# Kernel tuning notes

Hardware: AMD Instinct MI355X
Metric: run time of the kernel (lower is better)

Reference implementation:

```python
import jax, jax.numpy as jnp
import numpy as np

# Module constants (from init_kwargs)
WIN = 256      # window_size
STRIDE = 128   # stride (overlapping windows -> merge averages overlaps)
HEADS = 16


def setup_inputs() -> dict:
    key = jax.random.key(0)
    ks = jax.random.split(key, 5)
    B, S, D = 4, 4096, 1024
    scale = 0.02
    return {
        "hidden_states": jax.random.normal(ks[0], (B, S, D), jnp.float32),
        "Wq": jax.random.normal(ks[1], (D, D), jnp.float32) * scale,
        "Wk": jax.random.normal(ks[2], (D, D), jnp.float32) * scale,
        "Wv": jax.random.normal(ks[3], (D, D), jnp.float32) * scale,
        "Wo": jax.random.normal(ks[4], (D, D), jnp.float32) * scale,
    }


def reference(hidden_states, Wq, Wk, Wv, Wo):
    B, S, D = hidden_states.shape
    H = HEADS
    dh = D // H
    nw = (S - WIN) // STRIDE + 1  # number of sliding windows

    # gather overlapping windows: idx[w, j] = w*STRIDE + j
    idx = jnp.arange(nw)[:, None] * STRIDE + jnp.arange(WIN)[None, :]
    win = hidden_states[:, idx]

    # per-window multi-head attention (mask within a window is all-visible)
    def proj(x, Wm):
        return jnp.einsum('bnwd,de->bnwe', x, Wm).reshape(B, nw, WIN, H, dh)

    q = proj(win, Wq)
    k = proj(win, Wk)
    v = proj(win, Wv)

    scores = jnp.einsum('bnqhd,bnkhd->bnhqk', q, k) / jnp.sqrt(jnp.asarray(dh, q.dtype))
    attn = jax.nn.softmax(scores, axis=-1)
    ctx = jnp.einsum('bnhqk,bnkhd->bnqhd', attn, v)
    ctx = ctx.reshape(B, nw, WIN, D)
    win_out = jnp.einsum('bnwd,de->bnwe', ctx, Wo)

    # scatter-merge with overlap averaging
    flat_idx = idx.reshape(-1)
    out = jnp.zeros((B, S, D), hidden_states.dtype).at[:, flat_idx].add(
        win_out.reshape(B, nw * WIN, D))
    count = jnp.zeros((S,), hidden_states.dtype).at[flat_idx].add(1.0)
    out = out / (count[None, :, None] + 1e-8)
    return out
```

## Files before the change

kernel.cpp:

```cpp
#include <hip/hip_runtime.h>

#define SEQ 4096
#define DIM 1024
#define NWIN 31
#define NHEAD 16
#define NT 16

typedef __attribute__((ext_vector_type(8))) short bf16x8;
typedef __attribute__((ext_vector_type(4))) float f32x4;

#define MFMA(a, b, c) __builtin_amdgcn_mfma_f32_16x16x32_bf16((a), (b), (c), 0, 0, 0)

__device__ __forceinline__ unsigned short f2bf(float f) {
  union { float f; unsigned u; } v; v.f = f;
  unsigned r = v.u + 0x7FFFu + ((v.u >> 16) & 1u);
  return (unsigned short)(r >> 16);
}
__device__ __forceinline__ float bf2f(unsigned short h) {
  union { unsigned u; float f; } v; v.u = ((unsigned)h) << 16;
  return v.f;
}
__device__ __forceinline__ unsigned cvtpk(float lo, float hi) {
  unsigned r;
  asm("v_cvt_pk_bf16_f32 %0, %1, %2" : "=v"(r) : "v"(lo), "v"(hi));
  return r;
}
__device__ __forceinline__ unsigned addbf2(unsigned x, unsigned y) {
  union { unsigned u; float f; } a, b, c, d;
  a.u = x << 16; b.u = x & 0xffff0000u;
  c.u = y << 16; d.u = y & 0xffff0000u;
  return cvtpk(a.f + c.f, b.f + d.f);
}

__device__ __forceinline__ void gll16(const void* g, void* l) {
  __builtin_amdgcn_global_load_lds((const __attribute__((address_space(1))) unsigned*)g,
                                   (__attribute__((address_space(3))) unsigned*)l,
                                   16, 0, 0);
}


__global__ __launch_bounds__(256) void cast_x_k(const float* __restrict__ x,
                                                unsigned short* __restrict__ o) {
  size_t i = ((size_t)blockIdx.x * 256 + threadIdx.x) * 8;
  float4 a = *(const float4*)(x + i);
  float4 b = *(const float4*)(x + i + 4);
  union { unsigned short u[8]; uint4 v; } pk;
  pk.u[0] = f2bf(a.x); pk.u[1] = f2bf(a.y); pk.u[2] = f2bf(a.z); pk.u[3] = f2bf(a.w);
  pk.u[4] = f2bf(b.x); pk.u[5] = f2bf(b.y); pk.u[6] = f2bf(b.z); pk.u[7] = f2bf(b.w);
  *(uint4*)(o + i) = pk.v;
}

__global__ __launch_bounds__(256) void zero_ctxb_k(unsigned short* __restrict__ ctxB) {
  int gtid = blockIdx.x * 256 + threadIdx.x;
  int idx = gtid * 8;
  int srow = idx >> 10;
  int b = srow >> 8;
  int r = srow & 255;
  int seqrow = b * SEQ + ((r < 128) ? r : (3840 + r));
  uint4 z = {0, 0, 0, 0};
  *(uint4*)(ctxB + (size_t)seqrow * DIM + (idx & 1023)) = z;
}


__global__ __launch_bounds__(256) void tcast_w_k(const float* __restrict__ W0, const float* __restrict__ W1,
                                                 const float* __restrict__ W2, const float* __restrict__ W3,
                                                 unsigned short* __restrict__ Wt3,
                                                 unsigned short* __restrict__ WoT) {
  __shared__ float tile[64][65];
  const int bid = blockIdx.x;
  const int mat = bid >> 8;
  const int t = bid & 255;
  const int tr = (t >> 4) * 64, tc = (t & 15) * 64;
  const float* W = (mat == 0) ? W0 : (mat == 1) ? W1 : (mat == 2) ? W2 : W3;
  unsigned short* out = (mat < 3) ? (Wt3 + (size_t)mat * 1024 * 1024) : WoT;
  const float fscale = (mat == 0) ? 0.18033688011112042f : 1.0f;
  const int tid = threadIdx.x;
  const int rr = tid >> 4, cc = (tid & 15) << 2;
#pragma unroll
  for (int i = 0; i < 4; ++i) {
    int r = i * 16 + rr;
    float4 v = *(const float4*)(W + (size_t)(tr + r) * DIM + tc + cc);
    tile[r][cc] = v.x; tile[r][cc + 1] = v.y; tile[r][cc + 2] = v.z; tile[r][cc + 3] = v.w;
  }
  __syncthreads();
#pragma unroll
  for (int i = 0; i < 4; ++i) {
    int orow = i * 16 + rr;
    union { unsigned short u[4]; uint2 v; } pk;
#pragma unroll
    for (int j = 0; j < 4; ++j) pk.u[j] = f2bf(tile[cc + j][orow] * fscale);
    *(uint2*)(out + (size_t)(tc + orow) * DIM + tr + cc) = pk.v;
  }
}


__device__ __forceinline__ void stage_half(const unsigned short* __restrict__ src,
                                           int row0, int kcol0, char* slot, int tid) {
  const int w = tid >> 6;
  const int r0 = tid >> 2;
  const int c = (((tid & 3) ^ ((tid >> 3) & 3))) * 8;
  gll16(src + (size_t)(row0 + r0) * DIM + kcol0 + c, slot + w * 1024);
  gll16(src + (size_t)(row0 + 128 + r0) * DIM + kcol0 + c, slot + 8192 + w * 1024);
}

__device__ __forceinline__ void gemm256_core(const unsigned short* __restrict__ A,
                                             const unsigned short* __restrict__ Bt,
                                             int m0, int n0, char* lds,
                                             f32x4 acc[8][4], int tid) {
  const int lane = tid & 63, w = tid >> 6;
  const int wm = w >> 2, wn = w & 3;
  const int l15 = lane & 15, g = lane >> 4;
  const int gs = g ^ ((l15 >> 1) & 3);

#define ASLOT(b, kk) (lds + ((b) * 2 + (kk)) * 16384)
#define BSLOT(b, kk) (lds + 65536 + ((b) * 2 + (kk)) * 16384)

  const int aoff = (wm * 128 + l15) * 64 + gs * 16;
  const int boff = (wn * 64 + l15) * 64 + gs * 16;

  stage_half(A,  m0, 0,  ASLOT(0, 0), tid);
  stage_half(Bt, n0, 0,  BSLOT(0, 0), tid);
  stage_half(A,  m0, 32, ASLOT(0, 1), tid);
  stage_half(Bt, n0, 32, BSLOT(0, 1), tid);
  stage_half(A,  m0, 64, ASLOT(1, 0), tid);
  stage_half(Bt, n0, 64, BSLOT(1, 0), tid);
  asm volatile("s_waitcnt vmcnt(8)" ::: "memory");
  __builtin_amdgcn_s_barrier();

  for (int s = 0; s < NT; ++s) {
    const int b = s & 1, nb = b ^ 1;
    const int k1 = (s + 1 < NT ? s + 1 : NT - 1) * 64;
    const int k2 = (s + 2 < NT ? s + 2 : NT - 1) * 64;
    char* Ab0 = ASLOT(b, 0); char* Ab1 = ASLOT(b, 1);
    char* Bb0 = BSLOT(b, 0); char* Bb1 = BSLOT(b, 1);
    bf16x8 af[8], bq0, bq1;

#pragma unroll
    for (int mt = 0; mt < 8; ++mt) af[mt] = *(const bf16x8*)(Ab0 + aoff + mt * 1024);
    bq0 = *(const bf16x8*)(Bb0 + boff);
    bq1 = *(const bf16x8*)(Bb0 + boff + 1024);
    stage_half(A, m0, k1 + 32, ASLOT(nb, 1), tid);
    __builtin_amdgcn_s_barrier();
    __builtin_amdgcn_s_setprio(1);
#pragma unroll
    for (int mt = 0; mt < 8; ++mt) {
      acc[mt][0] = MFMA(af[mt], bq0, acc[mt][0]);
      acc[mt][1] = MFMA(af[mt], bq1, acc[mt][1]);
    }
    __builtin_amdgcn_s_setprio(0);

    bq0 = *(const bf16x8*)(Bb0 + boff + 2048);
    bq1 = *(const bf16x8*)(Bb0 + boff + 3072);
    stage_half(Bt, n0, k1 + 32, BSLOT(nb, 1), tid);
    asm volatile("s_waitcnt vmcnt(8)" ::: "memory");
    __builtin_amdgcn_s_barrier();
    __builtin_amdgcn_s_setprio(1);
#pragma unroll
    for (int mt = 0; mt < 8; ++mt) {
      acc[mt][2] = MFMA(af[mt], bq0, acc[mt][2]);
      acc[mt][3] = MFMA(af[mt], bq1, acc[mt][3]);
    }
    __builtin_amdgcn_s_setprio(0);

#pragma unroll
    for (int mt = 0; mt < 8; ++mt) af[mt] = *(const bf16x8*)(Ab1 + aoff + mt * 1024);
    bq0 = *(const bf16x8*)(Bb1 + boff);
    bq1 = *(const bf16x8*)(Bb1 + boff + 1024);
    stage_half(A, m0, k2, ASLOT(b, 0), tid);
    __builtin_amdgcn_s_barrier();
    __builtin_amdgcn_s_setprio(1);
#pragma unroll
    for (int mt = 0; mt < 8; ++mt) {
      acc[mt][0] = MFMA(af[mt], bq0, acc[mt][0]);
      acc[mt][1] = MFMA(af[mt], bq1, acc[mt][1]);
    }
    __builtin_amdgcn_s_setprio(0);

    bq0 = *(const bf16x8*)(Bb1 + boff + 2048);
    bq1 = *(const bf16x8*)(Bb1 + boff + 3072);
    stage_half(Bt, n0, k2, BSLOT(b, 0), tid);
    asm volatile("s_waitcnt vmcnt(8)" ::: "memory");
    __builtin_amdgcn_s_barrier();
    __builtin_amdgcn_s_setprio(1);
#pragma unroll
    for (int mt = 0; mt < 8; ++mt) {
      acc[mt][2] = MFMA(af[mt], bq0, acc[mt][2]);
      acc[mt][3] = MFMA(af[mt], bq1, acc[mt][3]);
    }
    __builtin_amdgcn_s_setprio(0);
  }
#undef ASLOT
#undef BSLOT
}


struct AR { uint4 a0, b0, a1, b1; };

__device__ __forceinline__ void issueA(const unsigned short* __restrict__ cA,
                                       const unsigned short* __restrict__ cB,
                                       int row0, int kcol0, int tid, AR& r) {
  const int r0 = tid >> 2;
  const int c = (((tid & 3) ^ ((tid >> 3) & 3))) * 8;
  const size_t o1 = (size_t)(row0 + r0) * DIM + kcol0 + c;
  const size_t o2 = (size_t)(row0 + 128 + r0) * DIM + kcol0 + c;
  r.a0 = *(const uint4*)(cA + o1);
  r.b0 = *(const uint4*)(cB + o1);
  r.a1 = *(const uint4*)(cA + o2);
  r.b1 = *(const uint4*)(cB + o2);
}

__device__ __forceinline__ void writeA(char* slot, int tid, const AR& r) {
  uint4 lo, hi;
  lo.x = addbf2(r.a0.x, r.b0.x); lo.y = addbf2(r.a0.y, r.b0.y);
  lo.z = addbf2(r.a0.z, r.b0.z); lo.w = addbf2(r.a0.w, r.b0.w);
  hi.x = addbf2(r.a1.x, r.b1.x); hi.y = addbf2(r.a1.y, r.b1.y);
  hi.z = addbf2(r.a1.z, r.b1.z); hi.w = addbf2(r.a1.w, r.b1.w);
  *(uint4*)(slot + tid * 16) = lo;
  *(uint4*)(slot + 8192 + tid * 16) = hi;
}

__device__ __forceinline__ void gemm256_core_sum(const unsigned short* __restrict__ cA,
                                                 const unsigned short* __restrict__ cB,
                                                 const unsigned short* __restrict__ Bt,
                                                 int m0, int n0, char* lds,
                                                 f32x4 acc[8][4], int tid) {
  const int lane = tid & 63, w = tid >> 6;
  const int wm = w >> 2, wn = w & 3;
  const int l15 = lane & 15, g = lane >> 4;
  const int gs = g ^ ((l15 >> 1) & 3);

#define ASLOT(b, kk) (lds + ((b) * 2 + (kk)) * 16384)
#define BSLOT(b, kk) (lds + 65536 + ((b) * 2 + (kk)) * 16384)

  const int aoff = (wm * 128 + l15) * 64 + gs * 16;
  const int boff = (wn * 64 + l15) * 64 + gs * 16;

  AR R0, R1;
  issueA(cA, cB, m0, 0, tid, R0);  writeA(ASLOT(0, 0), tid, R0);
  issueA(cA, cB, m0, 32, tid, R0); writeA(ASLOT(0, 1), tid, R0);
  issueA(cA, cB, m0, 64, tid, R0); writeA(ASLOT(1, 0), tid, R0);
  stage_half(Bt, n0, 0,  BSLOT(0, 0), tid);
  stage_half(Bt, n0, 32, BSLOT(0, 1), tid);
  stage_half(Bt, n0, 64, BSLOT(1, 0), tid);
  issueA(cA, cB, m0, 96, tid, R1);
  asm volatile("s_waitcnt vmcnt(8)" ::: "memory");
  asm volatile("s_waitcnt lgkmcnt(0)" ::: "memory");
  __builtin_amdgcn_s_barrier();

  for (int s = 0; s < NT; ++s) {
    const int b = s & 1, nb = b ^ 1;
    const int k1 = (s + 1 < NT ? s + 1 : NT - 1) * 64;
    const int k2 = (s + 2 < NT ? s + 2 : NT - 1) * 64;
    char* Ab0 = ASLOT(b, 0); char* Ab1 = ASLOT(b, 1);
    char* Bb0 = BSLOT(b, 0); char* Bb1 = BSLOT(b, 1);
    bf16x8 af[8], bq0, bq1;
    (void)k1;

    writeA(ASLOT(nb, 1), tid, R1);
    asm volatile("s_waitcnt lgkmcnt(0)" ::: "memory");
    issueA(cA, cB, m0, k2, tid, R0);
#pragma unroll
    for (int mt = 0; mt < 8; ++mt) af[mt] = *(const bf16x8*)(Ab0 + aoff + mt * 1024);
    bq0 = *(const bf16x8*)(Bb0 + boff);
    bq1 = *(const bf16x8*)(Bb0 + boff + 1024);
    __builtin_amdgcn_s_barrier();
    __builtin_amdgcn_s_setprio(1);
#pragma unroll
    for (int mt = 0; mt < 8; ++mt) {
      acc[mt][0] = MFMA(af[mt], bq0, acc[mt][0]);
      acc[mt][1] = MFMA(af[mt], bq1, acc[mt][1]);
    }
    __builtin_amdgcn_s_setprio(0);

    bq0 = *(const bf16x8*)(Bb0 + boff + 2048);
    bq1 = *(const bf16x8*)(Bb0 + boff + 3072);
    stage_half(Bt, n0, k1 + 32, BSLOT(nb, 1), tid);
    asm volatile("s_waitcnt vmcnt(8)" ::: "memory");
    __builtin_amdgcn_s_barrier();
    __builtin_amdgcn_s_setprio(1);
#pragma unroll
    for (int mt = 0; mt < 8; ++mt) {
      acc[mt][2] = MFMA(af[mt], bq0, acc[mt][2]);
      acc[mt][3] = MFMA(af[mt], bq1, acc[mt][3]);
    }
    __builtin_amdgcn_s_setprio(0);

    writeA(ASLOT(b, 0), tid, R0);
    asm volatile("s_waitcnt lgkmcnt(0)" ::: "memory");
    issueA(cA, cB, m0, k2 + 32, tid, R1);
#pragma unroll
    for (int mt = 0; mt < 8; ++mt) af[mt] = *(const bf16x8*)(Ab1 + aoff + mt * 1024);
    bq0 = *(const bf16x8*)(Bb1 + boff);
    bq1 = *(const bf16x8*)(Bb1 + boff + 1024);
    __builtin_amdgcn_s_barrier();
    __builtin_amdgcn_s_setprio(1);
#pragma unroll
    for (int mt = 0; mt < 8; ++mt) {
      acc[mt][0] = MFMA(af[mt], bq0, acc[mt][0]);
      acc[mt][1] = MFMA(af[mt], bq1, acc[mt][1]);
    }
    __builtin_amdgcn_s_setprio(0);

    bq0 = *(const bf16x8*)(Bb1 + boff + 2048);
    bq1 = *(const bf16x8*)(Bb1 + boff + 3072);
    stage_half(Bt, n0, k2, BSLOT(b, 0), tid);
    asm volatile("s_waitcnt vmcnt(8)" ::: "memory");
    __builtin_amdgcn_s_barrier();
    __builtin_amdgcn_s_setprio(1);
#pragma unroll
    for (int mt = 0; mt < 8; ++mt) {
      acc[mt][2] = MFMA(af[mt], bq0, acc[mt][2]);
      acc[mt][3] = MFMA(af[mt], bq1, acc[mt][3]);
    }
    __builtin_amdgcn_s_setprio(0);
  }
#undef ASLOT
#undef BSLOT
}


__global__ __launch_bounds__(512, 2) void gemm_qkv_k(const unsigned short* __restrict__ Xb,
                                                     const unsigned short* __restrict__ Wt3,
                                                     unsigned short* __restrict__ Qb,
                                                     unsigned short* __restrict__ Kb,
                                                     unsigned short* __restrict__ Vt) {
  __shared__ char lds[131072];
  const int nwg = 768;
  const int wg = blockIdx.x;
  const int swz = (wg & 7) * (nwg >> 3) + (wg >> 3);
  const int mtile = swz / 12, ntile = swz % 12;
  const int m0 = mtile * 256, n0 = ntile * 256;
  const int tid = threadIdx.x;

  f32x4 acc[8][4] = {};
  gemm256_core(Xb, Wt3, m0, n0, lds, acc, tid);

  const int lane = tid & 63, w = tid >> 6;
  const int wm = w >> 2, wn = w & 3;
  const int l15 = lane & 15, g = lane >> 4;
  const int mg0 = m0 + wm * 128;
  const int ng0 = n0 + wn * 64;

  if (n0 < 2048) {
    unsigned short* O = (n0 < 1024) ? Qb : Kb;
    const int nb = (n0 < 1024) ? 0 : 1024;
#pragma unroll
    for (int mt = 0; mt < 8; ++mt)
#pragma unroll
      for (int nt = 0; nt < 4; ++nt) {
        int ng = ng0 + nt * 16 + l15 - nb;
        int mg = mg0 + mt * 16 + g * 4;
#pragma unroll
        for (int r = 0; r < 4; ++r)
          O[(size_t)(mg + r) * DIM + ng] = f2bf(acc[mt][nt][r]);
      }
  } else {
#pragma unroll
    for (int mt = 0; mt < 8; ++mt)
#pragma unroll
      for (int nt = 0; nt < 4; ++nt) {
        int ng = ng0 + nt * 16 + l15 - 2048;
        int mg = mg0 + mt * 16 + g * 4;
        union { unsigned short u[4]; uint2 v; } pk;
#pragma unroll
        for (int r = 0; r < 4; ++r) pk.u[r] = f2bf(acc[mt][nt][r]);
        *(uint2*)(Vt + (size_t)ng * (4 * SEQ) + mg) = pk.v;
      }
  }
}


__global__ __launch_bounds__(512, 2) void gemm_out_k(const unsigned short* __restrict__ cA,
                                                     const unsigned short* __restrict__ cB,
                                                     const unsigned short* __restrict__ WoT,
                                                     float* __restrict__ out) {
  __shared__ char lds[131072];
  const int nwg = 256;
  const int wg = blockIdx.x;
  const int swz = (wg & 7) * (nwg >> 3) + (wg >> 3);
  const int mtile = swz >> 2, ntile = swz & 3;
  const int m0 = mtile * 256, n0 = ntile * 256;
  const int tid = threadIdx.x;

  f32x4 acc[8][4] = {};
  gemm256_core_sum(cA, cB, WoT, m0, n0, lds, acc, tid);

  const int lane = tid & 63, w = tid >> 6;
  const int wm = w >> 2, wn = w & 3;
  const int l15 = lane & 15, g = lane >> 4;
  const int mg0 = m0 + wm * 128;
  const int ng0 = n0 + wn * 64;
#pragma unroll
  for (int mt = 0; mt < 8; ++mt)
#pragma unroll
    for (int nt = 0; nt < 4; ++nt) {
      int ng = ng0 + nt * 16 + l15;
      int mg = mg0 + mt * 16 + g * 4;
#pragma unroll
      for (int r = 0; r < 4; ++r) {
        int m = mg + r;
        int s = m & (SEQ - 1);
        float scl = (s < 128 || s >= SEQ - 128) ? 1.0f : 0.5f;
        out[(size_t)m * DIM + ng] = acc[mt][nt][r] * scl;
      }
    }
}


__global__ __launch_bounds__(512, 4) void attn_k(const unsigned short* __restrict__ Qb,
                                                 const unsigned short* __restrict__ Kb,
                                                 const unsigned short* __restrict__ Vt,
                                                 unsigned short* __restrict__ ctxA,
                                                 unsigned short* __restrict__ ctxB) {
  __shared__ char Kls[32768];
  __shared__ char Vls[32768];

  const int bid = blockIdx.x;
  const int h = bid & 15;
  const int rem = bid >> 4;
  const int n = rem % NWIN;
  const int b = rem / NWIN;
  const int tid = threadIdx.x;
  const int lane = tid & 63;
  const int w = tid >> 6;
  const int l15 = lane & 15, g = lane >> 4;

  const size_t qkbase = ((size_t)b * SEQ + (size_t)n * 128) * DIM + h * 64;
  const int wdst = w * 1024;

  {
    const int kr0 = tid >> 3;
    const int ksc = ((tid & 7) ^ (kr0 & 7)) * 8;
    const unsigned short* kg = Kb + qkbase + (size_t)kr0 * DIM + ksc;
#pragma unroll
    for (int j = 0; j < 4; ++j)
      gll16(kg + (size_t)(64 * j) * DIM, Kls + 8192 * j + wdst);
  }
  {
    const int vr0 = tid >> 5;
    const int vsc = ((tid & 31) ^ (vr0 & 7)) * 8;
    const unsigned short* vg = Vt + (size_t)(h * 64 + vr0) * (4 * SEQ) +
                               (size_t)b * SEQ + n * 128 + vsc;
#pragma unroll
    for (int j = 0; j < 4; ++j)
      gll16(vg + (size_t)(16 * j) * (4 * SEQ), Vls + 8192 * j + wdst);
  }

  bf16x8 qf[2][2];
#pragma unroll
  for (int qt = 0; qt < 2; ++qt)
#pragma unroll
    for (int kf = 0; kf < 2; ++kf)
      qf[qt][kf] = *(const bf16x8*)(Qb + qkbase +
                                    (size_t)(w * 32 + qt * 16 + l15) * DIM + kf * 32 + g * 8);

  __syncthreads();

  f32x4 acc[2][4] = {};
  f32x4 psv[2] = {};

  for (int kc = 0; kc < 4; ++kc) {
    f32x4 s0[4] = {}, s1[4] = {};
    __builtin_amdgcn_s_setprio(1);
#pragma unroll
    for (int kt = 0; kt < 4; ++kt) {
      int row = kc * 64 + kt * 16 + l15;
      bf16x8 k0 = *(const bf16x8*)(Kls + row * 128 + ((g ^ (row & 7)) << 4));
      bf16x8 k1 = *(const bf16x8*)(Kls + row * 128 + (((4 + g) ^ (row & 7)) << 4));
      s0[kt] = MFMA(k0, qf[0][0], s0[kt]);
      s0[kt] = MFMA(k1, qf[0][1], s0[kt]);
      s1[kt] = MFMA(k0, qf[1][0], s1[kt]);
      s1[kt] = MFMA(k1, qf[1][1], s1[kt]);
    }
    __builtin_amdgcn_s_setprio(0);
#pragma unroll
    for (int kt = 0; kt < 4; ++kt) {
#pragma unroll
      for (int r = 0; r < 4; ++r) {
        s0[kt][r] = exp2f(s0[kt][r]);
        s1[kt][r] = exp2f(s1[kt][r]);
      }
      psv[0] += s0[kt];
      psv[1] += s1[kt];
    }
    union { unsigned u[4]; bf16x8 v; } pa[2][2];
#pragma unroll
    for (int c = 0; c < 2; ++c) {
      pa[0][c].u[0] = cvtpk(s0[2 * c][0], s0[2 * c][1]);
      pa[0][c].u[1] = cvtpk(s0[2 * c][2], s0[2 * c][3]);
      pa[0][c].u[2] = cvtpk(s0[2 * c + 1][0], s0[2 * c + 1][1]);
      pa[0][c].u[3] = cvtpk(s0[2 * c + 1][2], s0[2 * c + 1][3]);
      pa[1][c].u[0] = cvtpk(s1[2 * c][0], s1[2 * c][1]);
      pa[1][c].u[1] = cvtpk(s1[2 * c][2], s1[2 * c][3]);
      pa[1][c].u[2] = cvtpk(s1[2 * c + 1][0], s1[2 * c + 1][1]);
      pa[1][c].u[3] = cvtpk(s1[2 * c + 1][2], s1[2 * c + 1][3]);
    }
    __builtin_amdgcn_s_setprio(1);
#pragma unroll
    for (int c = 0; c < 2; ++c)
#pragma unroll
      for (int dt = 0; dt < 4; ++dt) {
        int row = dt * 16 + l15;
        int c16 = kc * 8 + c * 4 + (g >> 1);
        int off = (g & 1) * 8;
        union { uint2 u2[2]; bf16x8 v; } vv;
        vv.u2[0] = *(const uint2*)(Vls + row * 512 + ((c16 ^ (row & 7)) << 4) + off);
        vv.u2[1] = *(const uint2*)(Vls + row * 512 + (((c16 + 2) ^ (row & 7)) << 4) + off);
        acc[0][dt] = MFMA(vv.v, pa[0][c].v, acc[0][dt]);
        acc[1][dt] = MFMA(vv.v, pa[1][c].v, acc[1][dt]);
      }
    __builtin_amdgcn_s_setprio(0);
  }

  unsigned short* outb = (n & 1) ? ctxB : ctxA;
  const size_t obase = ((size_t)b * SEQ + (size_t)n * 128 + w * 32) * DIM + h * 64;
#pragma unroll
  for (int qt = 0; qt < 2; ++qt) {
    float ps = psv[qt][0] + psv[qt][1] + psv[qt][2] + psv[qt][3];
    ps += __shfl_xor(ps, 16);
    ps += __shfl_xor(ps, 32);
    float inv = 1.0f / ps;
#pragma unroll
    for (int dt = 0; dt < 4; ++dt) {
      union { unsigned short u[4]; uint2 v; } pk;
#pragma unroll
      for (int r = 0; r < 4; ++r) pk.u[r] = f2bf(acc[qt][dt][r] * inv);
      *(uint2*)(outb + obase + (size_t)(qt * 16 + l15) * DIM + dt * 16 + g * 4) = pk.v;
    }
  }
}


extern "C" void kernel_launch(void* const* d_in, const int* in_sizes, int n_in,
                              void* d_out, int out_size, void* d_ws, size_t ws_size,
                              hipStream_t stream) {
  const float* X  = (const float*)d_in[0];
  const float* Wq = (const float*)d_in[1];
  const float* Wk = (const float*)d_in[2];
  const float* Wv = (const float*)d_in[3];
  const float* Wo = (const float*)d_in[4];
  float* out = (float*)d_out;

  char* ws = (char*)d_ws;
  const size_t SZ = (size_t)4 * SEQ * DIM * 2;
  unsigned short* Xb   = (unsigned short*)(ws);
  unsigned short* Wt3  = (unsigned short*)(ws + SZ);
  unsigned short* WoT  = (unsigned short*)(ws + SZ + 6291456);
  unsigned short* Qb   = (unsigned short*)(ws + SZ + 8388608);
  unsigned short* Kb   = (unsigned short*)(ws + 2 * SZ + 8388608);
  unsigned short* Vt   = (unsigned short*)(ws + 3 * SZ + 8388608);
  unsigned short* ctxA = (unsigned short*)(ws + 4 * SZ + 8388608);
  unsigned short* ctxB = (unsigned short*)(ws + 5 * SZ + 8388608);

  zero_ctxb_k<<<512, 256, 0, stream>>>(ctxB);
  cast_x_k<<<8192, 256, 0, stream>>>(X, Xb);
  tcast_w_k<<<1024, 256, 0, stream>>>(Wq, Wk, Wv, Wo, Wt3, WoT);
  gemm_qkv_k<<<768, 512, 0, stream>>>(Xb, Wt3, Qb, Kb, Vt);
  attn_k<<<4 * NWIN * NHEAD, 512, 0, stream>>>(Qb, Kb, Vt, ctxA, ctxB);
  gemm_out_k<<<256, 512, 0, stream>>>(ctxA, ctxB, WoT, out);
}
```

Measured before the change: 251.2 us.

## Restructure GEMM main loop into four quadrant phases with full-K fragment reuse

Reorganizes the inner loop of both GEMM mainloops into four phases, each covering one output quadrant (4 M-tiles by 2 N-tiles) over both K halves, in place of two K-half passes over 8x2 fragments. This cuts register pressure for A fragments and adds explicit lgkmcnt waits and extra barriers around each phase. Global staging is interleaved per phase and the vmcnt thresholds change to match. It risks more barrier overhead and possible LDS race windows if the wait counts are wrong.

```diff
diff --git a/kernel.cpp b/kernel.cpp
--- a/kernel.cpp
+++ b/kernel.cpp
@@ -124,7 +124,7 @@
   stage_half(Bt, n0, 32, BSLOT(0, 1), tid);
   stage_half(A,  m0, 64, ASLOT(1, 0), tid);
   stage_half(Bt, n0, 64, BSLOT(1, 0), tid);
-  asm volatile("s_waitcnt vmcnt(8)" ::: "memory");
+  asm volatile("s_waitcnt vmcnt(4)" ::: "memory");
   __builtin_amdgcn_s_barrier();
 
   for (int s = 0; s < NT; ++s) {
@@ -133,61 +133,84 @@
     const int k2 = (s + 2 < NT ? s + 2 : NT - 1) * 64;
     char* Ab0 = ASLOT(b, 0); char* Ab1 = ASLOT(b, 1);
     char* Bb0 = BSLOT(b, 0); char* Bb1 = BSLOT(b, 1);
-    bf16x8 af[8], bq0, bq1;
-
-#pragma unroll
-    for (int mt = 0; mt < 8; ++mt) af[mt] = *(const bf16x8*)(Ab0 + aoff + mt * 1024);
-    bq0 = *(const bf16x8*)(Bb0 + boff);
-    bq1 = *(const bf16x8*)(Bb0 + boff + 1024);
+    bf16x8 af[4][2], bqA[2][2], bqB[2][2];
+
+#pragma unroll
+    for (int mt = 0; mt < 4; ++mt) {
+      af[mt][0] = *(const bf16x8*)(Ab0 + aoff + mt * 1024);
+      af[mt][1] = *(const bf16x8*)(Ab1 + aoff + mt * 1024);
+    }
+#pragma unroll
+    for (int nt = 0; nt < 2; ++nt) {
+      bqA[nt][0] = *(const bf16x8*)(Bb0 + boff + nt * 1024);
+      bqA[nt][1] = *(const bf16x8*)(Bb1 + boff + nt * 1024);
+    }
     stage_half(A, m0, k1 + 32, ASLOT(nb, 1), tid);
-    __builtin_amdgcn_s_barrier();
-    __builtin_amdgcn_s_setprio(1);
-#pragma unroll
-    for (int mt = 0; mt < 8; ++mt) {
-      acc[mt][0] = MFMA(af[mt], bq0, acc[mt][0]);
-      acc[mt][1] = MFMA(af[mt], bq1, acc[mt][1]);
-    }
-    __builtin_amdgcn_s_setprio(0);
-
-    bq0 = *(const bf16x8*)(Bb0 + boff + 2048);
-    bq1 = *(const bf16x8*)(Bb0 + boff + 3072);
+    asm volatile("s_waitcnt lgkmcnt(8)" ::: "memory");
+    __builtin_amdgcn_s_barrier();
+    asm volatile("s_waitcnt lgkmcnt(0)" ::: "memory");
+    __builtin_amdgcn_s_setprio(1);
+#pragma unroll
+    for (int mt = 0; mt < 4; ++mt)
+#pragma unroll
+      for (int nt = 0; nt < 2; ++nt) {
+        acc[mt][nt] = MFMA(af[mt][0], bqA[nt][0], acc[mt][nt]);
+        acc[mt][nt] = MFMA(af[mt][1], bqA[nt][1], acc[mt][nt]);
+      }
+    __builtin_amdgcn_s_setprio(0);
+    __builtin_amdgcn_s_barrier();
+
+#pragma unroll
+    for (int nt = 0; nt < 2; ++nt) {
+      bqB[nt][0] = *(const bf16x8*)(Bb0 + boff + (nt + 2) * 1024);
+      bqB[nt][1] = *(const bf16x8*)(Bb1 + boff + (nt + 2) * 1024);
+    }
     stage_half(Bt, n0, k1 + 32, BSLOT(nb, 1), tid);
-    asm volatile("s_waitcnt vmcnt(8)" ::: "memory");
-    __builtin_amdgcn_s_barrier();
-    __builtin_amdgcn_s_setprio(1);
-#pragma unroll
-    for (int mt = 0; mt < 8; ++mt) {
-      acc[mt][2] = MFMA(af[mt], bq0, acc[mt][2]);
-      acc[mt][3] = MFMA(af[mt], bq1, acc[mt][3]);
-    }
-    __builtin_amdgcn_s_setprio(0);
-
-#pragma unroll
-    for (int mt = 0; mt < 8; ++mt) af[mt] = *(const bf16x8*)(Ab1 + aoff + mt * 1024);
-    bq0 = *(const bf16x8*)(Bb1 + boff);
-    bq1 = *(const bf16x8*)(Bb1 + boff + 1024);
+    __builtin_amdgcn_s_barrier();
+    asm volatile("s_waitcnt lgkmcnt(0)" ::: "memory");
+    __builtin_amdgcn_s_setprio(1);
+#pragma unroll
+    for (int mt = 0; mt < 4; ++mt)
+#pragma unroll
+      for (int nt = 0; nt < 2; ++nt) {
+        acc[mt][nt + 2] = MFMA(af[mt][0], bqB[nt][0], acc[mt][nt + 2]);
+        acc[mt][nt + 2] = MFMA(af[mt][1], bqB[nt][1], acc[mt][nt + 2]);
+      }
+    __builtin_amdgcn_s_setprio(0);
+    __builtin_amdgcn_s_barrier();
+
+#pragma unroll
+    for (int mt = 0; mt < 4; ++mt) {
+      af[mt][0] = *(const bf16x8*)(Ab0 + aoff + (mt + 4) * 1024);
+      af[mt][1] = *(const bf16x8*)(Ab1 + aoff + (mt + 4) * 1024);
+    }
+    stage_half(Bt, n0, k2, BSLOT(b, 0), tid);
+    __builtin_amdgcn_s_barrier();
+    asm volatile("s_waitcnt lgkmcnt(0)" ::: "memory");
+    __builtin_amdgcn_s_setprio(1);
+#pragma unroll
+    for (int mt = 0; mt < 4; ++mt)
+#pragma unroll
+      for (int nt = 0; nt < 2; ++nt) {
+        acc[mt + 4][nt + 2] = MFMA(af[mt][0], bqB[nt][0], acc[mt + 4][nt + 2]);
+        acc[mt + 4][nt + 2] = MFMA(af[mt][1], bqB[nt][1], acc[mt + 4][nt + 2]);
+      }
+    __builtin_amdgcn_s_setprio(0);
+    __builtin_amdgcn_s_barrier();
+
     stage_half(A, m0, k2, ASLOT(b, 0), tid);
-    __builtin_amdgcn_s_barrier();
-    __builtin_amdgcn_s_setprio(1);
-#pragma unroll
-    for (int mt = 0; mt < 8; ++mt) {
-      acc[mt][0] = MFMA(af[mt], bq0, acc[mt][0]);
-      acc[mt][1] = MFMA(af[mt], bq1, acc[mt][1]);
-    }
-    __builtin_amdgcn_s_setprio(0);
-
-    bq0 = *(const bf16x8*)(Bb1 + boff + 2048);
-    bq1 = *(const bf16x8*)(Bb1 + boff + 3072);
-    stage_half(Bt, n0, k2, BSLOT(b, 0), tid);
-    asm volatile("s_waitcnt vmcnt(8)" ::: "memory");
-    __builtin_amdgcn_s_barrier();
-    __builtin_amdgcn_s_setprio(1);
-#pragma unroll
-    for (int mt = 0; mt < 8; ++mt) {
-      acc[mt][2] = MFMA(af[mt], bq0, acc[mt][2]);
-      acc[mt][3] = MFMA(af[mt], bq1, acc[mt][3]);
-    }
-    __builtin_amdgcn_s_setprio(0);
+    asm volatile("s_waitcnt vmcnt(4)" ::: "memory");
+    __builtin_amdgcn_s_barrier();
+    __builtin_amdgcn_s_setprio(1);
+#pragma unroll
+    for (int mt = 0; mt < 4; ++mt)
+#pragma unroll
+      for (int nt = 0; nt < 2; ++nt) {
+        acc[mt + 4][nt] = MFMA(af[mt][0], bqA[nt][0], acc[mt + 4][nt]);
+        acc[mt + 4][nt] = MFMA(af[mt][1], bqA[nt][1], acc[mt + 4][nt]);
+      }
+    __builtin_amdgcn_s_setprio(0);
+    __builtin_amdgcn_s_barrier();
   }
 #undef ASLOT
 #undef BSLOT
@@ -243,8 +266,8 @@
   stage_half(Bt, n0, 32, BSLOT(0, 1), tid);
   stage_half(Bt, n0, 64, BSLOT(1, 0), tid);
   issueA(cA, cB, m0, 96, tid, R1);
-  asm volatile("s_waitcnt vmcnt(8)" ::: "memory");
   asm volatile("s_waitcnt lgkmcnt(0)" ::: "memory");
+  asm volatile("s_waitcnt vmcnt(6)" ::: "memory");
   __builtin_amdgcn_s_barrier();
 
   for (int s = 0; s < NT; ++s) {
@@ -253,66 +276,87 @@
     const int k2 = (s + 2 < NT ? s + 2 : NT - 1) * 64;
     char* Ab0 = ASLOT(b, 0); char* Ab1 = ASLOT(b, 1);
     char* Bb0 = BSLOT(b, 0); char* Bb1 = BSLOT(b, 1);
-    bf16x8 af[8], bq0, bq1;
-    (void)k1;
+    bf16x8 af[4][2], bqA[2][2], bqB[2][2];
 
     writeA(ASLOT(nb, 1), tid, R1);
     asm volatile("s_waitcnt lgkmcnt(0)" ::: "memory");
     issueA(cA, cB, m0, k2, tid, R0);
 #pragma unroll
-    for (int mt = 0; mt < 8; ++mt) af[mt] = *(const bf16x8*)(Ab0 + aoff + mt * 1024);
-    bq0 = *(const bf16x8*)(Bb0 + boff);
-    bq1 = *(const bf16x8*)(Bb0 + boff + 1024);
-    __builtin_amdgcn_s_barrier();
-    __builtin_amdgcn_s_setprio(1);
-#pragma unroll
-    for (int mt = 0; mt < 8; ++mt) {
-      acc[mt][0] = MFMA(af[mt], bq0, acc[mt][0]);
-      acc[mt][1] = MFMA(af[mt], bq1, acc[mt][1]);
-    }
-    __builtin_amdgcn_s_setprio(0);
-
-    bq0 = *(const bf16x8*)(Bb0 + boff + 2048);
-    bq1 = *(const bf16x8*)(Bb0 + boff + 3072);
+    for (int mt = 0; mt < 4; ++mt) {
+      af[mt][0] = *(const bf16x8*)(Ab0 + aoff + mt * 1024);
+      af[mt][1] = *(const bf16x8*)(Ab1 + aoff + mt * 1024);
+    }
+#pragma unroll
+    for (int nt = 0; nt < 2; ++nt) {
+      bqA[nt][0] = *(const bf16x8*)(Bb0 + boff + nt * 1024);
+      bqA[nt][1] = *(const bf16x8*)(Bb1 + boff + nt * 1024);
+    }
+    __builtin_amdgcn_s_barrier();
+    asm volatile("s_waitcnt lgkmcnt(0)" ::: "memory");
+    __builtin_amdgcn_s_setprio(1);
+#pragma unroll
+    for (int mt = 0; mt < 4; ++mt)
+#pragma unroll
+      for (int nt = 0; nt < 2; ++nt) {
+        acc[mt][nt] = MFMA(af[mt][0], bqA[nt][0], acc[mt][nt]);
+        acc[mt][nt] = MFMA(af[mt][1], bqA[nt][1], acc[mt][nt]);
+      }
+    __builtin_amdgcn_s_setprio(0);
+    __builtin_amdgcn_s_barrier();
+
+#pragma unroll
+    for (int nt = 0; nt < 2; ++nt) {
+      bqB[nt][0] = *(const bf16x8*)(Bb0 + boff + (nt + 2) * 1024);
+      bqB[nt][1] = *(const bf16x8*)(Bb1 + boff + (nt + 2) * 1024);
+    }
     stage_half(Bt, n0, k1 + 32, BSLOT(nb, 1), tid);
-    asm volatile("s_waitcnt vmcnt(8)" ::: "memory");
-    __builtin_amdgcn_s_barrier();
-    __builtin_amdgcn_s_setprio(1);
-#pragma unroll
-    for (int mt = 0; mt < 8; ++mt) {
-      acc[mt][2] = MFMA(af[mt], bq0, acc[mt][2]);
-      acc[mt][3] = MFMA(af[mt], bq1, acc[mt][3]);
-    }
-    __builtin_amdgcn_s_setprio(0);
+    __builtin_amdgcn_s_barrier();
+    asm volatile("s_waitcnt lgkmcnt(0)" ::: "memory");
+    __builtin_amdgcn_s_setprio(1);
+#pragma unroll
+    for (int mt = 0; mt < 4; ++mt)
+#pragma unroll
+      for (int nt = 0; nt < 2; ++nt) {
+        acc[mt][nt + 2] = MFMA(af[mt][0], bqB[nt][0], acc[mt][nt + 2]);
+        acc[mt][nt + 2] = MFMA(af[mt][1], bqB[nt][1], acc[mt][nt + 2]);
+      }
+    __builtin_amdgcn_s_setprio(0);
+    __builtin_amdgcn_s_barrier();
+
+    issueA(cA, cB, m0, k2 + 32, tid, R1);
+#pragma unroll
+    for (int mt = 0; mt < 4; ++mt) {
+      af[mt][0] = *(const bf16x8*)(Ab0 + aoff + (mt + 4) * 1024);
+      af[mt][1] = *(const bf16x8*)(Ab1 + aoff + (mt + 4) * 1024);
+    }
+    stage_half(Bt, n0, k2, BSLOT(b, 0), tid);
+    __builtin_amdgcn_s_barrier();
+    asm volatile("s_waitcnt lgkmcnt(0)" ::: "memory");
+    __builtin_amdgcn_s_setprio(1);
+#pragma unroll
+    for (int mt = 0; mt < 4; ++mt)
+#pragma unroll
+      for (int nt = 0; nt < 2; ++nt) {
+        acc[mt + 4][nt + 2] = MFMA(af[mt][0], bqB[nt][0], acc[mt + 4][nt + 2]);
+        acc[mt + 4][nt + 2] = MFMA(af[mt][1], bqB[nt][1], acc[mt + 4][nt + 2]);
+      }
+    __builtin_amdgcn_s_setprio(0);
+    __builtin_amdgcn_s_barrier();
 
     writeA(ASLOT(b, 0), tid, R0);
     asm volatile("s_waitcnt lgkmcnt(0)" ::: "memory");
-    issueA(cA, cB, m0, k2 + 32, tid, R1);
-#pragma unroll
-    for (int mt = 0; mt < 8; ++mt) af[mt] = *(const bf16x8*)(Ab1 + aoff + mt * 1024);
-    bq0 = *(const bf16x8*)(Bb1 + boff);
-    bq1 = *(const bf16x8*)(Bb1 + boff + 1024);
-    __builtin_amdgcn_s_barrier();
-    __builtin_amdgcn_s_setprio(1);
-#pragma unroll
-    for (int mt = 0; mt < 8; ++mt) {
-      acc[mt][0] = MFMA(af[mt], bq0, acc[mt][0]);
-      acc[mt][1] = MFMA(af[mt], bq1, acc[mt][1]);
-    }
-    __builtin_amdgcn_s_setprio(0);
-
-    bq0 = *(const bf16x8*)(Bb1 + boff + 2048);
-    bq1 = *(const bf16x8*)(Bb1 + boff + 3072);
-    stage_half(Bt, n0, k2, BSLOT(b, 0), tid);
-    asm volatile("s_waitcnt vmcnt(8)" ::: "memory");
-    __builtin_amdgcn_s_barrier();
-    __builtin_amdgcn_s_setprio(1);
-#pragma unroll
-    for (int mt = 0; mt < 8; ++mt) {
-      acc[mt][2] = MFMA(af[mt], bq0, acc[mt][2]);
-      acc[mt][3] = MFMA(af[mt], bq1, acc[mt][3]);
-    }
-    __builtin_amdgcn_s_setprio(0);
+    asm volatile("s_waitcnt vmcnt(6)" ::: "memory");
+    __builtin_amdgcn_s_barrier();
+    __builtin_amdgcn_s_setprio(1);
+#pragma unroll
+    for (int mt = 0; mt < 4; ++mt)
+#pragma unroll
+      for (int nt = 0; nt < 2; ++nt) {
+        acc[mt + 4][nt] = MFMA(af[mt][0], bqA[nt][0], acc[mt + 4][nt]);
+        acc[mt + 4][nt] = MFMA(af[mt][1], bqA[nt][1], acc[mt + 4][nt]);
+      }
+    __builtin_amdgcn_s_setprio(0);
+    __builtin_amdgcn_s_barrier();
   }
 #undef ASLOT
 #undef BSLOT
```

Measured after the change: 262.5 us. 4.5% more time.
